# Performance work log

Measured on AMD Instinct MI355X. Metric: run time of the kernel, lower is better.

## Reference

```python
import jax, jax.numpy as jnp
import numpy as np

jax.config.update("jax_enable_x64", True)  # torch uses double for the scale decomposition

ACC = 23  # 'accuracy' in integer_multiply_shift_round


def _fixed_point_mul(x_int, new_scale):
    """Bit-exact integer multiply-shift-round: x * new_scale where
    new_scale = m * 2**e (frexp), m quantized to ACC-bit integer mantissa."""
    m, e = jnp.frexp(new_scale)                      # m in [0.5, 1)
    nm = jnp.round(m * (1 << ACC)).astype(jnp.int64)  # torch casts to int32 (ACC<32); int64 is a safe superset
    tmp = x_int.astype(jnp.int64) * nm                # [B,S,D] int64
    e = e.astype(jnp.int64)
    sl = jnp.maximum(e - ACC, 0)                      # left-shift amount (e - ACC >= 0 branch)
    sr = jnp.maximum(ACC - e, 0)                      # right-shift amount (sr_round_na branch)
    left = tmp << sl
    bit = (tmp < 0).astype(jnp.int64)
    nudge = (jnp.int64(1) << jnp.maximum(sr - 1, 0)) - bit   # round-half-away-from-zero nudge
    right = jnp.where(sr > 0, (tmp + nudge) >> sr, tmp)      # sr==0 -> identity (sr_round_na early return)
    return jnp.where(e - ACC >= 0, left, right)


def setup_inputs() -> dict:
    key = jax.random.key(0)
    k1, k2 = jax.random.split(key)
    B, S, D = 4, 4096, 2048
    # integer-valued pre-activations (int32 accumulators), stored as float32 holding exact ints
    x = jax.random.randint(k1, (B, S, D), -2048, 2048, dtype=jnp.int32).astype(jnp.float32)
    identity = jax.random.randint(k2, (B, S, D), -2048, 2048, dtype=jnp.int32).astype(jnp.float32)
    return {
        "x": x,
        "identity": identity,
        "pre_act_scaling_factor": jnp.array([0.004], jnp.float32),
        "identity_scaling_factor": jnp.array([0.002], jnp.float32),
        "x_min": jnp.array([-8.0], jnp.float32),   # calibrated activation range buffers
        "x_max": jnp.array([8.0], jnp.float32),
    }


def reference(x, identity, pre_act_scaling_factor, identity_scaling_factor, x_min, x_max):
    bit = 8
    n = 2 ** (bit - 1) - 1  # 127
    # symmetric_linear_quantization_params (per-tensor)
    scale = jnp.clip(jnp.maximum(jnp.abs(x_min), jnp.abs(x_max)), 1e-8, None) / n  # [1] float32
    # FixedPointMul: requantize pre_act and identity to the output scale, add, clamp
    s64 = scale.astype(jnp.float64)
    ns_x = pre_act_scaling_factor.astype(jnp.float64) / s64
    ns_id = identity_scaling_factor.astype(jnp.float64) / s64
    out = _fixed_point_mul(x.astype(jnp.int64), ns_x) + _fixed_point_mul(identity.astype(jnp.int64), ns_id)
    q = jnp.clip(out, -n - 1, n).astype(jnp.int8)  # bit_num<=8 -> int8
    # QuantAct returns dequantized activation and its scale
    return q.astype(jnp.float32) * scale.astype(jnp.float32), scale
```

## Files before the change

### kernel.cpp

```cpp
#include <hip/hip_runtime.h>
#include <math.h>

#define ACC_BITS 23

struct QParams {
    float scale;
    int   fast;
    int   nmx_hi, nmx_lo, Kx, srx12;
    int   nmi_hi, nmi_lo, Ki, sri12;
    long long nm_x64, nm_i64;
    int   e_x, e_i;
};

__global__ void qparams_kernel(const float* __restrict__ pre_sf,
                               const float* __restrict__ id_sf,
                               const float* __restrict__ xminp,
                               const float* __restrict__ xmaxp,
                               QParams* __restrict__ p,
                               float* __restrict__ out_scale)
{
    float s = fmaxf(fmaxf(fabsf(xminp[0]), fabsf(xmaxp[0])), 1e-8f);
    float scale = s / 127.0f;

    double s64  = (double)scale;
    double ns_x = (double)pre_sf[0] / s64;
    double ns_i = (double)id_sf[0] / s64;

    int e_x, e_i;
    double m_x = frexp(ns_x, &e_x);
    double m_i = frexp(ns_i, &e_i);
    long long nm_x = (long long)rint(m_x * 8388608.0);
    long long nm_i = (long long)rint(m_i * 8388608.0);

    p->scale  = scale;
    p->nm_x64 = nm_x;  p->e_x = e_x;
    p->nm_i64 = nm_i;  p->e_i = e_i;

    long long ax = nm_x, ai = nm_i;
    int ex = e_x, ei = e_i;
    if (ax == (1LL << 23)) { ax >>= 1; ex += 1; }
    if (ai == (1LL << 23)) { ai >>= 1; ei += 1; }
    int sr_x = ACC_BITS - ex, sr_i = ACC_BITS - ei;

    int fast = (ax > 0) && (ax < (1LL << 23)) &&
               (ai > 0) && (ai < (1LL << 23)) &&
               (sr_x >= 12) && (sr_x <= 30) && (sr_i >= 12) && (sr_i <= 30);
    p->fast = fast;
    p->nmx_hi = (int)(ax >> 12); p->nmx_lo = (int)(ax & 0xFFF);
    p->nmi_hi = (int)(ai >> 12); p->nmi_lo = (int)(ai & 0xFFF);
    p->Kx = fast ? (1 << (sr_x - 1)) : 0;
    p->Ki = fast ? (1 << (sr_i - 1)) : 0;
    p->srx12 = sr_x - 12;
    p->sri12 = sr_i - 12;

    *out_scale = scale;
}

__device__ __forceinline__ long long fixed_point_mul64(long long xi, long long nm, int e) {
    long long tmp = xi * nm;
    if (e - ACC_BITS >= 0) {
        return tmp << (e - ACC_BITS);
    } else {
        int sr = ACC_BITS - e;
        long long nudge = (1LL << (sr - 1)) - (long long)(tmp < 0);
        return (tmp + nudge) >> sr;
    }
}

__device__ __forceinline__ int fpm24(int xi, int nm_hi, int nm_lo, int K, int sr12) {
    int bit = (int)((unsigned)xi >> 31);
    int B = (__mul24(xi, nm_lo) + K - bit) >> 12;
    int A = __mul24(xi, nm_hi);
    return (A + B) >> sr12;
}

typedef float f32x4 __attribute__((ext_vector_type(4)));

#define TPB   256
#define VPT   4
#define TILE  (TPB * VPT)

__global__ void __launch_bounds__(TPB)
quantact_main(const f32x4* __restrict__ x,
              const f32x4* __restrict__ idn,
              f32x4* __restrict__ out,
              const QParams* __restrict__ p,
              int n4, int n)
{
    const float scale = p->scale;
    const int base = blockIdx.x * TILE + threadIdx.x;

    if (p->fast) {
        const int nmx_hi = p->nmx_hi, nmx_lo = p->nmx_lo, Kx = p->Kx, srx = p->srx12;
        const int nmi_hi = p->nmi_hi, nmi_lo = p->nmi_lo, Ki = p->Ki, sri = p->sri12;

        if (base + (VPT - 1) * TPB < n4) {
            f32x4 xv[VPT], iv[VPT];
            #pragma unroll
            for (int k = 0; k < VPT; ++k) xv[k] = x[base + k * TPB];
            #pragma unroll
            for (int k = 0; k < VPT; ++k) iv[k] = idn[base + k * TPB];

            f32x4 ov[VPT];
            #pragma unroll
            for (int k = 0; k < VPT; ++k) {
                #pragma unroll
                for (int c = 0; c < 4; ++c) {
                    int o = fpm24((int)xv[k][c], nmx_hi, nmx_lo, Kx, srx)
                          + fpm24((int)iv[k][c], nmi_hi, nmi_lo, Ki, sri);
                    o = o < -128 ? -128 : (o > 127 ? 127 : o);
                    ov[k][c] = (float)o * scale;
                }
            }
            #pragma unroll
            for (int k = 0; k < VPT; ++k) out[base + k * TPB] = ov[k];
        } else {
            #pragma unroll
            for (int k = 0; k < VPT; ++k) {
                int i = base + k * TPB;
                if (i < n4) {
                    f32x4 xv = x[i], iv = idn[i], ov;
                    #pragma unroll
                    for (int c = 0; c < 4; ++c) {
                        int o = fpm24((int)xv[c], nmx_hi, nmx_lo, Kx, srx)
                              + fpm24((int)iv[c], nmi_hi, nmi_lo, Ki, sri);
                        o = o < -128 ? -128 : (o > 127 ? 127 : o);
                        ov[c] = (float)o * scale;
                    }
                    out[i] = ov;
                }
            }
        }
    } else {
        const long long nm64_x = p->nm_x64, nm64_i = p->nm_i64;
        const int e_x = p->e_x, e_i = p->e_i;
        #pragma unroll
        for (int k = 0; k < VPT; ++k) {
            int i = base + k * TPB;
            if (i < n4) {
                f32x4 xv = x[i], iv = idn[i], ov;
                #pragma unroll
                for (int c = 0; c < 4; ++c) {
                    long long o = fixed_point_mul64((long long)xv[c], nm64_x, e_x)
                                + fixed_point_mul64((long long)iv[c], nm64_i, e_i);
                    o = o < -128 ? -128 : (o > 127 ? 127 : o);
                    ov[c] = (float)(int)o * scale;
                }
                out[i] = ov;
            }
        }
    }

    if (blockIdx.x == 0) {
        const float* xs  = (const float*)x;
        const float* is_ = (const float*)idn;
        float* os = (float*)out;
        const long long nm64_x = p->nm_x64, nm64_i = p->nm_i64;
        const int e_x = p->e_x, e_i = p->e_i;
        for (int j = n4 * 4 + (int)threadIdx.x; j < n; j += TPB) {
            long long o = fixed_point_mul64((long long)xs[j], nm64_x, e_x)
                        + fixed_point_mul64((long long)is_[j], nm64_i, e_i);
            o = o < -128 ? -128 : (o > 127 ? 127 : o);
            os[j] = (float)(int)o * scale;
        }
    }
}

extern "C" void kernel_launch(void* const* d_in, const int* in_sizes, int n_in,
                              void* d_out, int out_size, void* d_ws, size_t ws_size,
                              hipStream_t stream) {
    const f32x4* x      = (const f32x4*)d_in[0];
    const f32x4* idn    = (const f32x4*)d_in[1];
    const float* pre_sf = (const float*)d_in[2];
    const float* id_sf  = (const float*)d_in[3];
    const float* xmin   = (const float*)d_in[4];
    const float* xmax   = (const float*)d_in[5];

    int n  = in_sizes[0];
    int n4 = n / 4;

    float* out       = (float*)d_out;
    float* out_scale = out + n;
    QParams* p       = (QParams*)d_ws;

    qparams_kernel<<<1, 1, 0, stream>>>(pre_sf, id_sf, xmin, xmax, p, out_scale);

    int grid = (n4 + TILE - 1) / TILE;
    if (grid < 1) grid = 1;
    quantact_main<<<grid, TPB, 0, stream>>>(x, idn, (f32x4*)out, p, n4, n);
}
```

Before: 316.5 us.

## Fuse qparams computation into main kernel and use nontemporal stores

Removes the single-thread qparams kernel launch and its workspace round-trip by having every thread recompute the quantization parameters redundantly from the scalar inputs. The bulk loads are issued before that scalar computation so it can overlap with memory latency, and output stores become nontemporal to reduce cache pollution. The cost is redundant double-precision frexp and divide work in every thread, plus a larger register footprint.

```diff
diff --git a/kernel.cpp b/kernel.cpp
--- a/kernel.cpp
+++ b/kernel.cpp
@@ -3,7 +3,13 @@
 
 #define ACC_BITS 23
 
-struct QParams {
+typedef float f32x4 __attribute__((ext_vector_type(4)));
+
+#define TPB   256
+#define VPT   4
+#define TILE  (TPB * VPT)
+
+struct QP {
     float scale;
     int   fast;
     int   nmx_hi, nmx_lo, Kx, srx12;
@@ -12,19 +18,15 @@
     int   e_x, e_i;
 };
 
-__global__ void qparams_kernel(const float* __restrict__ pre_sf,
-                               const float* __restrict__ id_sf,
-                               const float* __restrict__ xminp,
-                               const float* __restrict__ xmaxp,
-                               QParams* __restrict__ p,
-                               float* __restrict__ out_scale)
-{
-    float s = fmaxf(fmaxf(fabsf(xminp[0]), fabsf(xmaxp[0])), 1e-8f);
+__device__ __forceinline__ QP compute_qparams(float pre, float idsf,
+                                              float xmn, float xmx) {
+    QP q;
+    float s     = fmaxf(fmaxf(fabsf(xmn), fabsf(xmx)), 1e-8f);
     float scale = s / 127.0f;
 
     double s64  = (double)scale;
-    double ns_x = (double)pre_sf[0] / s64;
-    double ns_i = (double)id_sf[0] / s64;
+    double ns_x = (double)pre  / s64;
+    double ns_i = (double)idsf / s64;
 
     int e_x, e_i;
     double m_x = frexp(ns_x, &e_x);
@@ -32,9 +34,9 @@
     long long nm_x = (long long)rint(m_x * 8388608.0);
     long long nm_i = (long long)rint(m_i * 8388608.0);
 
-    p->scale  = scale;
-    p->nm_x64 = nm_x;  p->e_x = e_x;
-    p->nm_i64 = nm_i;  p->e_i = e_i;
+    q.scale  = scale;
+    q.nm_x64 = nm_x;  q.e_x = e_x;
+    q.nm_i64 = nm_i;  q.e_i = e_i;
 
     long long ax = nm_x, ai = nm_i;
     int ex = e_x, ei = e_i;
@@ -42,18 +44,16 @@
     if (ai == (1LL << 23)) { ai >>= 1; ei += 1; }
     int sr_x = ACC_BITS - ex, sr_i = ACC_BITS - ei;
 
-    int fast = (ax > 0) && (ax < (1LL << 23)) &&
-               (ai > 0) && (ai < (1LL << 23)) &&
-               (sr_x >= 12) && (sr_x <= 30) && (sr_i >= 12) && (sr_i <= 30);
-    p->fast = fast;
-    p->nmx_hi = (int)(ax >> 12); p->nmx_lo = (int)(ax & 0xFFF);
-    p->nmi_hi = (int)(ai >> 12); p->nmi_lo = (int)(ai & 0xFFF);
-    p->Kx = fast ? (1 << (sr_x - 1)) : 0;
-    p->Ki = fast ? (1 << (sr_i - 1)) : 0;
-    p->srx12 = sr_x - 12;
-    p->sri12 = sr_i - 12;
-
-    *out_scale = scale;
+    q.fast = (ax > 0) && (ax < (1LL << 23)) &&
+             (ai > 0) && (ai < (1LL << 23)) &&
+             (sr_x >= 12) && (sr_x <= 30) && (sr_i >= 12) && (sr_i <= 30);
+    q.nmx_hi = (int)(ax >> 12); q.nmx_lo = (int)(ax & 0xFFF);
+    q.nmi_hi = (int)(ai >> 12); q.nmi_lo = (int)(ai & 0xFFF);
+    q.Kx = q.fast ? (1 << (sr_x - 1)) : 0;
+    q.Ki = q.fast ? (1 << (sr_i - 1)) : 0;
+    q.srx12 = sr_x - 12;
+    q.sri12 = sr_i - 12;
+    return q;
 }
 
 __device__ __forceinline__ long long fixed_point_mul64(long long xi, long long nm, int e) {
@@ -74,33 +74,39 @@
     return (A + B) >> sr12;
 }
 
-typedef float f32x4 __attribute__((ext_vector_type(4)));
+__global__ void __launch_bounds__(TPB)
+quantact_fused(const f32x4* __restrict__ x,
+               const f32x4* __restrict__ idn,
+               f32x4* __restrict__ out,
+               float* __restrict__ out_scale,
+               const float* __restrict__ pre_sf,
+               const float* __restrict__ id_sf,
+               const float* __restrict__ xminp,
+               const float* __restrict__ xmaxp,
+               int n4, int n)
+{
+    const int base = blockIdx.x * TILE + (int)threadIdx.x;
+    const bool full = (base + (VPT - 1) * TPB) < n4;
 
-#define TPB   256
-#define VPT   4
-#define TILE  (TPB * VPT)
+    f32x4 xv[VPT], iv[VPT];
+    if (full) {
+        #pragma unroll
+        for (int k = 0; k < VPT; ++k) {
+            xv[k] = x  [base + k * TPB];
+            iv[k] = idn[base + k * TPB];
+        }
+    }
 
-__global__ void __launch_bounds__(TPB)
-quantact_main(const f32x4* __restrict__ x,
-              const f32x4* __restrict__ idn,
-              f32x4* __restrict__ out,
-              const QParams* __restrict__ p,
-              int n4, int n)
-{
-    const float scale = p->scale;
-    const int base = blockIdx.x * TILE + threadIdx.x;
+    const QP q = compute_qparams(pre_sf[0], id_sf[0], xminp[0], xmaxp[0]);
+    const float scale = q.scale;
 
-    if (p->fast) {
-        const int nmx_hi = p->nmx_hi, nmx_lo = p->nmx_lo, Kx = p->Kx, srx = p->srx12;
-        const int nmi_hi = p->nmi_hi, nmi_lo = p->nmi_lo, Ki = p->Ki, sri = p->sri12;
+    if (blockIdx.x == 0 && threadIdx.x == 0) *out_scale = scale;
 
-        if (base + (VPT - 1) * TPB < n4) {
-            f32x4 xv[VPT], iv[VPT];
-            #pragma unroll
-            for (int k = 0; k < VPT; ++k) xv[k] = x[base + k * TPB];
-            #pragma unroll
-            for (int k = 0; k < VPT; ++k) iv[k] = idn[base + k * TPB];
+    if (q.fast) {
+        const int nmx_hi = q.nmx_hi, nmx_lo = q.nmx_lo, Kx = q.Kx, srx = q.srx12;
+        const int nmi_hi = q.nmi_hi, nmi_lo = q.nmi_lo, Ki = q.Ki, sri = q.sri12;
 
+        if (full) {
             f32x4 ov[VPT];
             #pragma unroll
             for (int k = 0; k < VPT; ++k) {
@@ -113,40 +119,43 @@
                 }
             }
             #pragma unroll
-            for (int k = 0; k < VPT; ++k) out[base + k * TPB] = ov[k];
+            for (int k = 0; k < VPT; ++k)
+                __builtin_nontemporal_store(ov[k], &out[base + k * TPB]);
         } else {
             #pragma unroll
             for (int k = 0; k < VPT; ++k) {
                 int i = base + k * TPB;
                 if (i < n4) {
-                    f32x4 xv = x[i], iv = idn[i], ov;
+                    f32x4 xw = x[i], iw = idn[i], ov;
                     #pragma unroll
                     for (int c = 0; c < 4; ++c) {
-                        int o = fpm24((int)xv[c], nmx_hi, nmx_lo, Kx, srx)
-                              + fpm24((int)iv[c], nmi_hi, nmi_lo, Ki, sri);
+                        int o = fpm24((int)xw[c], nmx_hi, nmx_lo, Kx, srx)
+                              + fpm24((int)iw[c], nmi_hi, nmi_lo, Ki, sri);
                         o = o < -128 ? -128 : (o > 127 ? 127 : o);
                         ov[c] = (float)o * scale;
                     }
-                    out[i] = ov;
+                    __builtin_nontemporal_store(ov, &out[i]);
                 }
             }
         }
     } else {
-        const long long nm64_x = p->nm_x64, nm64_i = p->nm_i64;
-        const int e_x = p->e_x, e_i = p->e_i;
+        const long long nm64_x = q.nm_x64, nm64_i = q.nm_i64;
+        const int e_x = q.e_x, e_i = q.e_i;
         #pragma unroll
         for (int k = 0; k < VPT; ++k) {
             int i = base + k * TPB;
             if (i < n4) {
-                f32x4 xv = x[i], iv = idn[i], ov;
+                f32x4 xw, iw, ov;
+                if (full) { xw = xv[k]; iw = iv[k]; }
+                else      { xw = x[i];  iw = idn[i]; }
                 #pragma unroll
                 for (int c = 0; c < 4; ++c) {
-                    long long o = fixed_point_mul64((long long)xv[c], nm64_x, e_x)
-                                + fixed_point_mul64((long long)iv[c], nm64_i, e_i);
+                    long long o = fixed_point_mul64((long long)xw[c], nm64_x, e_x)
+                                + fixed_point_mul64((long long)iw[c], nm64_i, e_i);
                     o = o < -128 ? -128 : (o > 127 ? 127 : o);
                     ov[c] = (float)(int)o * scale;
                 }
-                out[i] = ov;
+                __builtin_nontemporal_store(ov, &out[i]);
             }
         }
     }
@@ -155,8 +164,8 @@
         const float* xs  = (const float*)x;
         const float* is_ = (const float*)idn;
         float* os = (float*)out;
-        const long long nm64_x = p->nm_x64, nm64_i = p->nm_i64;
-        const int e_x = p->e_x, e_i = p->e_i;
+        const long long nm64_x = q.nm_x64, nm64_i = q.nm_i64;
+        const int e_x = q.e_x, e_i = q.e_i;
         for (int j = n4 * 4 + (int)threadIdx.x; j < n; j += TPB) {
             long long o = fixed_point_mul64((long long)xs[j], nm64_x, e_x)
                         + fixed_point_mul64((long long)is_[j], nm64_i, e_i);
@@ -181,11 +190,9 @@
 
     float* out       = (float*)d_out;
     float* out_scale = out + n;
-    QParams* p       = (QParams*)d_ws;
-
-    qparams_kernel<<<1, 1, 0, stream>>>(pre_sf, id_sf, xmin, xmax, p, out_scale);
 
     int grid = (n4 + TILE - 1) / TILE;
     if (grid < 1) grid = 1;
-    quantact_main<<<grid, TPB, 0, stream>>>(x, idn, (f32x4*)out, p, n4, n);
+    quantact_fused<<<grid, TPB, 0, stream>>>(x, idn, (f32x4*)out, out_scale,
+                                             pre_sf, id_sf, xmin, xmax, n4, n);
 }
```

New measurement: 325.9 us. 1.03x slower.
